# Optimization experiments

Hardware: AMD Instinct MI355X
Metric: run time of the kernel (lower is better)

## Reference

```python
import jax, jax.numpy as jnp
import numpy as np

H, KVH, HD = 32, 8, 128          # query heads, kv heads, head_dim
HIDDEN = H * HD                   # 4096
TOTAL_KV = 3072                   # sum of (start_pos + seqlen) over the batch (static)
ROPE_THETA = 10000.0


def setup_inputs() -> dict:
    key = jax.random.key(0)
    ks = jax.random.split(key, 4)
    x = jax.random.normal(ks[0], (1024, HIDDEN), jnp.float32)
    wqkv = jax.random.normal(ks[1], (HIDDEN, HIDDEN + 2 * KVH * HD), jnp.float32) * 0.02
    wo = jax.random.normal(ks[2], (HIDDEN, HIDDEN), jnp.float32) * 0.02
    # paged cache: [num_layers=1, 2(k/v), cache_slots, kv_heads, head_dim], holds post-RoPE prefixes
    kv_cache = jax.random.normal(ks[3], (1, 2, 8192, KVH, HD), jnp.float32) * 0.02
    # 4 ragged requests: seqlens [512,256,128,128], cached prefixes [0,512,1024,512]
    seqstarts = jnp.array([0, 512, 768, 896, 1024], jnp.int32)
    start_pos = jnp.array([0, 512, 1024, 512], jnp.int32)
    kvstarts = jnp.array([0, 512, 1280, 2432, 3072], jnp.int32)  # cumsum of start_pos+seqlen
    cachestarts = jnp.array([0, 1024, 2560, 4096], jnp.int32)    # page base per request
    return dict(x=x, wqkv=wqkv, wo=wo, kv_cache=kv_cache, seqstarts=seqstarts,
                kvstarts=kvstarts, cachestarts=cachestarts, start_pos=start_pos)


def _rope(t, pos):
    # interleaved (GPT-J style) rotary over full head_dim; t: [T, nheads, HD], pos: [T]
    d2 = HD // 2
    inv_freq = 1.0 / (ROPE_THETA ** (jnp.arange(d2, dtype=jnp.float32) / d2))
    ang = pos.astype(jnp.float32)[:, None] * inv_freq      # [T, d2]
    cos = jnp.cos(ang)[:, None, :]
    sin = jnp.sin(ang)[:, None, :]
    x1, x2 = t[..., 0::2], t[..., 1::2]
    r1 = x1 * cos - x2 * sin
    r2 = x1 * sin + x2 * cos
    return jnp.stack([r1, r2], axis=-1).reshape(t.shape)


def _forward(x, wqkv, wo, kv_cache, seqstarts, kvstarts, cachestarts, start_pos):
    T = x.shape[0]
    # fused QKV projection
    xqkv = (x @ wqkv).reshape(T, H + 2 * KVH, HD)
    xq, xk, xv = jnp.split(xqkv, [H, H + KVH], axis=1)   # [T,32,HD],[T,8,HD],[T,8,HD]

    # per-token batch id and absolute position (ragged via seqstarts)
    tok = jnp.arange(T)
    bq = jnp.searchsorted(seqstarts, tok, side='right') - 1
    pos_q = tok - seqstarts[bq] + start_pos[bq]
    xq = _rope(xq, pos_q)
    xk = _rope(xk, pos_q)

    # assemble ragged KV stream: cached prefix (paged cache) + freshly projected tokens
    kvtok = jnp.arange(TOTAL_KV)
    bkv = jnp.searchsorted(kvstarts, kvtok, side='right') - 1
    pkv = kvtok - kvstarts[bkv]                              # absolute kv position
    is_new = pkv >= start_pos[bkv]
    new_idx = jnp.clip(seqstarts[bkv] + pkv - start_pos[bkv], 0, T - 1)
    cache_idx = cachestarts[bkv] + pkv                       # paged slot for prefix
    keys = jnp.where(is_new[:, None, None], xk[new_idx], kv_cache[0, 0][cache_idx])
    vals = jnp.where(is_new[:, None, None], xv[new_idx], kv_cache[0, 1][cache_idx])

    # GQA: repeat kv heads to match query heads
    rep = H // KVH
    keys = jnp.repeat(keys, rep, axis=1)                     # [TOTAL_KV, 32, HD]
    vals = jnp.repeat(vals, rep, axis=1)

    scale = 1.0 / jnp.sqrt(jnp.float32(HD))
    scores = jnp.einsum('qhd,khd->hqk', xq, keys) * scale    # [32, T, TOTAL_KV]
    # ragged causal mask: same request and kv position <= query position
    mask = (bq[:, None] == bkv[None, :]) & (pkv[None, :] <= pos_q[:, None])
    scores = jnp.where(mask[None], scores, jnp.float32(-1e30))
    probs = jax.nn.softmax(scores, axis=-1)
    attn = jnp.einsum('hqk,khd->qhd', probs, vals)           # [T, 32, HD]
    return attn.reshape(T, HIDDEN) @ wo


def reference(x, wqkv, wo, kv_cache, seqstarts, kvstarts, cachestarts, start_pos):
    return _forward(x, wqkv, wo, kv_cache, seqstarts, kvstarts, cachestarts, start_pos)
```

## Files before the change

### kernel.cpp

```cpp
#include <hip/hip_runtime.h>
#include <hip/hip_bf16.h>
#include <math.h>
#include <stdint.h>

typedef __bf16 bf16;
typedef __attribute__((ext_vector_type(4))) float floatx4;
typedef __attribute__((ext_vector_type(8))) bf16 bf16x8;
typedef __attribute__((ext_vector_type(4))) bf16 bf16x4;

#define LDS_ASYNC16(gptr, lptr)                                                \
  __builtin_amdgcn_global_load_lds(                                            \
      (const __attribute__((address_space(1))) void*)(gptr),                   \
      (__attribute__((address_space(3))) void*)(lptr), 16, 0, 0)

__global__ __launch_bounds__(256) void k_merge(const float* __restrict__ a,
                                               const float* __restrict__ b,
                                               float* __restrict__ out) {
  int i = (blockIdx.x * 256 + threadIdx.x) * 4;
  float4 va = *(const float4*)(a + i);
  float4 vb = *(const float4*)(b + i);
  float4 o;
  o.x = va.x + vb.x; o.y = va.y + vb.y; o.z = va.z + vb.z; o.w = va.w + vb.w;
  *(float4*)(out + i) = o;
}

__device__ __forceinline__ void transpose_tile(const float* __restrict__ in,
                                               bf16* __restrict__ out, int K,
                                               int N, int bx, int by, int tid,
                                               float (*tile)[65]) {
  int k0 = by * 64, n0 = bx * 64;
  int cg = tid & 15, rr = tid >> 4;
#pragma unroll
  for (int p = 0; p < 4; ++p) {
    int r = rr + p * 16;
    float4 v = *(const float4*)(in + (size_t)(k0 + r) * N + n0 + cg * 4);
    tile[r][cg * 4 + 0] = v.x; tile[r][cg * 4 + 1] = v.y;
    tile[r][cg * 4 + 2] = v.z; tile[r][cg * 4 + 3] = v.w;
  }
  __syncthreads();
  int kc = tid & 7;
#pragma unroll
  for (int p = 0; p < 2; ++p) {
    int n = (tid >> 3) + p * 32;
    bf16x8 o;
#pragma unroll
    for (int e = 0; e < 8; ++e) o[e] = (bf16)tile[kc * 8 + e][n];
    *(bf16x8*)(out + (size_t)(n0 + n) * K + k0 + kc * 8) = o;
  }
}

__global__ __launch_bounds__(256) void k_prep(const float* __restrict__ x,
                                              const float* __restrict__ wqkv,
                                              const float* __restrict__ wo,
                                              bf16* __restrict__ x_bf,
                                              bf16* __restrict__ wqkvT,
                                              bf16* __restrict__ woT) {
  __shared__ float tile[64][65];
  int bid = blockIdx.x, tid = threadIdx.x;
  if (bid < 2048) {
    int i = (bid * 256 + tid) * 8;
    float4 a = *(const float4*)(x + i);
    float4 b = *(const float4*)(x + i + 4);
    bf16x8 o;
    o[0] = (bf16)a.x; o[1] = (bf16)a.y; o[2] = (bf16)a.z; o[3] = (bf16)a.w;
    o[4] = (bf16)b.x; o[5] = (bf16)b.y; o[6] = (bf16)b.z; o[7] = (bf16)b.w;
    *(bf16x8*)(x_bf + i) = o;
  } else if (bid < 8192) {
    int q = bid - 2048;
    transpose_tile(wqkv, wqkvT, 4096, 6144, q >> 6, q & 63, tid, tile);
  } else {
    int q = bid - 8192;
    transpose_tile(wo, woT, 4096, 4096, q >> 6, q & 63, tid, tile);
  }
}

__global__ __launch_bounds__(256) void k_gemm_bt(const bf16* __restrict__ A,
                                                 const bf16* __restrict__ B,
                                                 float* __restrict__ C,
                                                 int M, int N, int K, int ksplit) {
  __shared__ bf16 As[128 * 32];
  __shared__ bf16 Bs[128 * 32];
  int tid = threadIdx.x;
  int w = tid >> 6, lane = tid & 63;
  int lq = lane >> 4, l16 = lane & 15;
  int bm = blockIdx.y * 128, bn = blockIdx.x * 128;
  int wm = (w >> 1) * 64, wn = (w & 1) * 64;
  int kc = K / ksplit;
  int koff = blockIdx.z * kc;
  C += (size_t)blockIdx.z * M * N;
  floatx4 acc[4][4] = {};
  const bf16* Ab = A + (size_t)bm * K;
  const bf16* Bb = B + (size_t)bn * K;
  int srow = (lane >> 2);
  int scol = (((lane & 3) ^ ((srow >> 1) & 3))) * 8;
  int sa = (l16 >> 1) & 3;

  for (int k0 = koff; k0 < koff + kc; k0 += 32) {
#pragma unroll
    for (int c = 0; c < 2; ++c) {
      int r = w * 32 + c * 16 + srow;
      LDS_ASYNC16(Ab + (size_t)r * K + k0 + scol, &As[(w * 32 + c * 16) * 32]);
      LDS_ASYNC16(Bb + (size_t)r * K + k0 + scol, &Bs[(w * 32 + c * 16) * 32]);
    }
    __syncthreads();
    bf16x8 af[4], bfr[4];
#pragma unroll
    for (int i = 0; i < 4; ++i)
      af[i] = *(const bf16x8*)&As[(wm + i * 16 + l16) * 32 + (lq ^ sa) * 8];
#pragma unroll
    for (int j = 0; j < 4; ++j)
      bfr[j] = *(const bf16x8*)&Bs[(wn + j * 16 + l16) * 32 + (lq ^ sa) * 8];
#pragma unroll
    for (int i = 0; i < 4; ++i)
#pragma unroll
      for (int j = 0; j < 4; ++j)
        acc[i][j] = __builtin_amdgcn_mfma_f32_16x16x32_bf16(af[i], bfr[j],
                                                            acc[i][j], 0, 0, 0);
    __syncthreads();
  }
#pragma unroll
  for (int i = 0; i < 4; ++i)
#pragma unroll
    for (int j = 0; j < 4; ++j) {
      int m = bm + wm + i * 16 + lq * 4;
      int n = bn + wn + j * 16 + l16;
      float* cp = C + (size_t)m * N + n;
#pragma unroll
      for (int r = 0; r < 4; ++r) cp[(size_t)r * N] = acc[i][j][r];
    }
}

__global__ __launch_bounds__(256) void k_rope_asm(
    const float* __restrict__ xp0, const float* __restrict__ xp1,
    bf16* __restrict__ qb, bf16* __restrict__ kall, bf16* __restrict__ vT,
    const float* __restrict__ ck, const float* __restrict__ cv,
    const int* __restrict__ seqstarts, const int* __restrict__ kvstarts,
    const int* __restrict__ cachestarts, const int* __restrict__ start_pos) {
  __shared__ float tile[64][130];
  int bid = blockIdx.x, tid = threadIdx.x;
  if (bid < 1024) {
    int t = bid;
    int s = 0;
    for (int i = 1; i < 4; ++i) if (seqstarts[i] <= t) s = i;
    int posn = t - seqstarts[s] + start_pos[s];
    float pos = (float)posn;
    int krow = kvstarts[s] + posn;
    for (int wk = tid; wk < 40 * 64; wk += 256) {
      int hh = wk >> 6, j = wk & 63;
      size_t idx = ((size_t)t * 48 + hh) * 128 + 2 * j;
      float2 a0 = *(const float2*)(xp0 + idx);
      float2 a1 = *(const float2*)(xp1 + idx);
      float x1 = a0.x + a1.x;
      float x2 = a0.y + a1.y;
      float invf = exp2f(-(float)j * 0.20762050593045935f);
      float ang = pos * invf;
      float sv, cv2;
      sincosf(ang, &sv, &cv2);
      float r1 = x1 * cv2 - x2 * sv;
      float r2 = x1 * sv + x2 * cv2;
      unsigned int u1 = (unsigned int)__builtin_bit_cast(unsigned short, (bf16)r1);
      unsigned int u2 = (unsigned int)__builtin_bit_cast(unsigned short, (bf16)r2);
      unsigned int pk = u1 | (u2 << 16);
      unsigned int* dst = (hh < 32)
          ? (unsigned int*)(qb + ((size_t)t * 32 + hh) * 128)
          : (unsigned int*)(kall + ((size_t)(hh - 32) * 3072 + krow) * 128);
      dst[j] = pk;
    }
    return;
  }
  int rb = bid - 1024;
  if (rb < 3072) {
    int p = rb;
    int b = 0;
    for (int i = 1; i < 4; ++i) if (kvstarts[i] <= p) b = i;
    int pkv = p - kvstarts[b];
    if (pkv >= start_pos[b]) return;
    int hk = tid >> 5, d4 = (tid & 31) * 4;
    int ci = cachestarts[b] + pkv;
    float4 v = *(const float4*)(ck + ((size_t)ci * 8 + hk) * 128 + d4);
    bf16x4 o;
    o[0] = (bf16)v.x; o[1] = (bf16)v.y; o[2] = (bf16)v.z; o[3] = (bf16)v.w;
    *(bf16x4*)(kall + ((size_t)hk * 3072 + p) * 128 + d4) = o;
    return;
  }
  int q = rb - 3072;
  int hk = q / 48, p0 = (q % 48) * 64;
  {
    int r = tid >> 2;
    int p = p0 + r;
    int b = 0;
    for (int i = 1; i < 4; ++i) if (kvstarts[i] <= p) b = i;
    int pkv = p - kvstarts[b];
    int f0 = (tid & 3) * 32;
    if (pkv >= start_pos[b]) {
      int tn = seqstarts[b] + pkv - start_pos[b];
      size_t base = (size_t)tn * 6144 + (40 + hk) * 128;
#pragma unroll
      for (int i = 0; i < 8; ++i) {
        float4 v0 = *(const float4*)(xp0 + base + f0 + i * 4);
        float4 v1 = *(const float4*)(xp1 + base + f0 + i * 4);
        tile[r][f0 + i * 4 + 0] = v0.x + v1.x;
        tile[r][f0 + i * 4 + 1] = v0.y + v1.y;
        tile[r][f0 + i * 4 + 2] = v0.z + v1.z;
        tile[r][f0 + i * 4 + 3] = v0.w + v1.w;
      }
    } else {
      int ci = cachestarts[b] + pkv;
      const float* src = cv + ((size_t)ci * 8 + hk) * 128;
#pragma unroll
      for (int i = 0; i < 8; ++i) {
        float4 v = *(const float4*)(src + f0 + i * 4);
        tile[r][f0 + i * 4 + 0] = v.x; tile[r][f0 + i * 4 + 1] = v.y;
        tile[r][f0 + i * 4 + 2] = v.z; tile[r][f0 + i * 4 + 3] = v.w;
      }
    }
  }
  __syncthreads();
  int d = tid >> 1, hf = tid & 1;
  bf16* dst = vT + ((size_t)hk * 128 + d) * 3072 + p0 + hf * 32;
#pragma unroll
  for (int qq = 0; qq < 4; ++qq) {
    bf16x8 o;
#pragma unroll
    for (int e = 0; e < 8; ++e) o[e] = (bf16)tile[hf * 32 + qq * 8 + e][d];
    *(bf16x8*)(dst + qq * 8) = o;
  }
}

__global__ __launch_bounds__(256) void k_attn(
    const bf16* __restrict__ qb, const bf16* __restrict__ kall,
    const bf16* __restrict__ vT, bf16* __restrict__ aout,
    const int* __restrict__ seqstarts, const int* __restrict__ kvstarts,
    const int* __restrict__ start_pos) {
  __shared__ bf16 Ks[64 * 128];
  __shared__ bf16 Vs[128 * 64];
  __shared__ bf16 Ps[64 * 64];
  int bid = blockIdx.x;
  int half = bid >> 8, idx = bid & 255;
  int h = half * 16 + (idx >> 4);
  int qbi = half ? (idx & 15) : 15 - (idx & 15);
  int hk = h >> 2;
  int t0 = qbi * 64;
  int s = 0;
  for (int i = 1; i < 4; ++i) if (seqstarts[i] <= t0) s = i;
  int posbase = t0 - seqstarts[s] + start_pos[s];
  int kv0 = kvstarts[s];
  int nkv = posbase + 64;
  int tid = threadIdx.x, w = tid >> 6, lane = tid & 63;
  int lq = lane >> 4, l16 = lane & 15;

  bf16x8 qa[4];
#pragma unroll
  for (int kk = 0; kk < 4; ++kk)
    qa[kk] = *(const bf16x8*)(qb + (((size_t)(t0 + w * 16 + l16) * 32 + h) * 128 +
                                    kk * 32 + lq * 8));

  int krow = lane >> 4;
  int vrow = lane >> 3;
  int vchunk = ((lane & 7) ^ (vrow & 7));
  int sw8 = l16 & 7;

  float m_r[4], l_r[4];
  floatx4 oacc[8] = {};
#pragma unroll
  for (int rg = 0; rg < 4; ++rg) { m_r[rg] = -3.0e38f; l_r[rg] = 0.f; }
  const float scale = 0.08838834764831845f;

  for (int p0 = 0; p0 < nkv; p0 += 64) {
#pragma unroll
    for (int c = 0; c < 4; ++c) {
      int base_r = w * 16 + c * 4;
      int r = base_r + krow;
      int gch = (lane & 15) ^ ((c * 4 + krow) & 15);
      LDS_ASYNC16(kall + (((size_t)hk * 3072 + kv0 + p0 + r) * 128 + gch * 8),
                  &Ks[base_r * 128]);
    }
#pragma unroll
    for (int c = 0; c < 4; ++c) {
      int base_d = w * 32 + c * 8;
      int d = base_d + vrow;
      LDS_ASYNC16(vT + (((size_t)hk * 128 + d) * 3072 + kv0 + p0 + vchunk * 8),
                  &Vs[base_d * 64]);
    }
    __syncthreads();

    floatx4 sacc[4] = {};
#pragma unroll
    for (int kk = 0; kk < 4; ++kk)
#pragma unroll
      for (int j = 0; j < 4; ++j) {
        bf16x8 kb = *(const bf16x8*)&Ks[(j * 16 + l16) * 128 +
                                        ((kk * 4 + lq) ^ l16) * 8];
        sacc[j] = __builtin_amdgcn_mfma_f32_16x16x32_bf16(qa[kk], kb, sacc[j], 0, 0, 0);
      }

#pragma unroll
    for (int rg = 0; rg < 4; ++rg) {
      int qpos = posbase + w * 16 + lq * 4 + rg;
      float sv[4];
      float rmax = -3.0e38f;
#pragma unroll
      for (int j = 0; j < 4; ++j) {
        int pkv = p0 + j * 16 + l16;
        sv[j] = (pkv <= qpos) ? sacc[j][rg] * scale : -3.0e38f;
        rmax = fmaxf(rmax, sv[j]);
      }
#pragma unroll
      for (int off = 1; off < 16; off <<= 1)
        rmax = fmaxf(rmax, __shfl_xor(rmax, off, 64));
      float mnew = fmaxf(m_r[rg], rmax);
      float alpha = __expf(m_r[rg] - mnew);
      m_r[rg] = mnew;
      int prow = w * 16 + lq * 4 + rg;
      int pswz = (lq * 4 + rg) & 7;
      float psum = 0.f;
#pragma unroll
      for (int j = 0; j < 4; ++j) {
        float pv = __expf(sv[j] - mnew);
        psum += pv;
        int chunk = (j * 2 + (l16 >> 3)) ^ pswz;
        Ps[prow * 64 + chunk * 8 + (l16 & 7)] = (bf16)pv;
      }
#pragma unroll
      for (int off = 1; off < 16; off <<= 1) psum += __shfl_xor(psum, off, 64);
      l_r[rg] = l_r[rg] * alpha + psum;
#pragma unroll
      for (int nt = 0; nt < 8; ++nt) oacc[nt][rg] *= alpha;
    }

#pragma unroll
    for (int kk = 0; kk < 2; ++kk) {
      bf16x8 pa = *(const bf16x8*)&Ps[(w * 16 + l16) * 64 +
                                      ((kk * 4 + lq) ^ sw8) * 8];
#pragma unroll
      for (int nt = 0; nt < 8; ++nt) {
        bf16x8 vb = *(const bf16x8*)&Vs[(nt * 16 + l16) * 64 +
                                        ((kk * 4 + lq) ^ sw8) * 8];
        oacc[nt] = __builtin_amdgcn_mfma_f32_16x16x32_bf16(pa, vb, oacc[nt], 0, 0, 0);
      }
    }
    __syncthreads();
  }

#pragma unroll
  for (int rg = 0; rg < 4; ++rg) {
    int row = w * 16 + lq * 4 + rg;
    float inv = 1.0f / l_r[rg];
    bf16* dst = aout + (size_t)(t0 + row) * 4096 + h * 128;
#pragma unroll
    for (int nt = 0; nt < 8; ++nt)
      dst[nt * 16 + l16] = (bf16)(oacc[nt][rg] * inv);
  }
}

extern "C" void kernel_launch(void* const* d_in, const int* in_sizes, int n_in,
                              void* d_out, int out_size, void* d_ws, size_t ws_size,
                              hipStream_t stream) {
  const float* x = (const float*)d_in[0];
  const float* wqkv = (const float*)d_in[1];
  const float* wo = (const float*)d_in[2];
  const float* kv = (const float*)d_in[3];
  const int* seqstarts = (const int*)d_in[4];
  const int* kvstarts = (const int*)d_in[5];
  const int* cachestarts = (const int*)d_in[6];
  const int* start_pos = (const int*)d_in[7];
  float* out = (float*)d_out;

  char* base = (char*)d_ws;
  size_t off = 0;
  auto carve = [&](size_t bytes) {
    void* r = base + off;
    off += (bytes + 255) & ~(size_t)255;
    return r;
  };
  bf16* x_bf    = (bf16*)carve(1024ull * 4096 * 2);
  bf16* wqkvT   = (bf16*)carve(6144ull * 4096 * 2);
  bf16* woT     = (bf16*)carve(4096ull * 4096 * 2);
  float* xqkv   = (float*)carve(2ull * 1024 * 6144 * 4);
  bf16* q_bf    = (bf16*)carve(1024ull * 32 * 128 * 2);
  bf16* k_all   = (bf16*)carve(8ull * 3072 * 128 * 2);
  bf16* vT_all  = (bf16*)carve(8ull * 128 * 3072 * 2);
  bf16* attn_bf = (bf16*)carve(1024ull * 4096 * 2);
  float* outp = (float*)wqkvT;

  float* xqkv1 = xqkv + 1024ull * 6144;
  const float* cache_v = kv + 8192ull * 8 * 128;

  k_prep<<<12288, 256, 0, stream>>>(x, wqkv, wo, x_bf, wqkvT, woT);
  k_gemm_bt<<<dim3(48, 8, 2), 256, 0, stream>>>(x_bf, wqkvT, xqkv, 1024, 6144,
                                                4096, 2);
  k_rope_asm<<<4480, 256, 0, stream>>>(xqkv, xqkv1, q_bf, k_all, vT_all, kv,
                                       cache_v, seqstarts, kvstarts,
                                       cachestarts, start_pos);
  k_attn<<<512, 256, 0, stream>>>(q_bf, k_all, vT_all, attn_bf,
                                  seqstarts, kvstarts, start_pos);
  k_gemm_bt<<<dim3(32, 8, 2), 256, 0, stream>>>(attn_bf, woT, outp, 1024, 4096,
                                                4096, 2);
  k_merge<<<4096, 256, 0, stream>>>(outp, outp + 1024ull * 4096, out);
}
```

Measured before the change: 474.8 us.

## Widen weight transpose tiles and split attention into 32-row query blocks

The weight transpose in the prep kernel now handles 64x128 tiles per block, with all global loads batched into registers before the LDS writes and narrower bf16x4 stores on the way out. The attention kernel drops to 128 threads (2 waves) per block over 32-query tiles, doubling the grid to 1024 blocks and reordering them so heavy query tiles start first. This aims for better load balance and occupancy in attention and fewer, larger transpose blocks. The risks are that the narrower bf16x4 stores coalesce less well, and that each block now loads the full K/V tiles for only 32 queries, so K/V reuse per block halves.

Result: no change. 474.9 us (+0.0%).

```diff
diff --git a/kernel.cpp b/kernel.cpp
--- a/kernel.cpp
+++ b/kernel.cpp
@@ -24,28 +24,38 @@
   *(float4*)(out + i) = o;
 }
 
-__device__ __forceinline__ void transpose_tile(const float* __restrict__ in,
-                                               bf16* __restrict__ out, int K,
-                                               int N, int bx, int by, int tid,
-                                               float (*tile)[65]) {
-  int k0 = by * 64, n0 = bx * 64;
+__device__ __forceinline__ void transpose_tile128(const float* __restrict__ in,
+                                                  bf16* __restrict__ out, int K,
+                                                  int N, int bx, int by, int tid,
+                                                  float (*tile)[129]) {
+  int k0 = by * 64, n0 = bx * 128;
   int cg = tid & 15, rr = tid >> 4;
-#pragma unroll
-  for (int p = 0; p < 4; ++p) {
-    int r = rr + p * 16;
-    float4 v = *(const float4*)(in + (size_t)(k0 + r) * N + n0 + cg * 4);
-    tile[r][cg * 4 + 0] = v.x; tile[r][cg * 4 + 1] = v.y;
-    tile[r][cg * 4 + 2] = v.z; tile[r][cg * 4 + 3] = v.w;
-  }
+  float4 v[8];
+#pragma unroll
+  for (int p = 0; p < 4; ++p)
+#pragma unroll
+    for (int h = 0; h < 2; ++h)
+      v[p * 2 + h] = *(const float4*)(in + (size_t)(k0 + rr + p * 16) * N +
+                                      n0 + h * 64 + cg * 4);
+#pragma unroll
+  for (int p = 0; p < 4; ++p)
+#pragma unroll
+    for (int h = 0; h < 2; ++h) {
+      float4 t = v[p * 2 + h];
+      int r = rr + p * 16, c = h * 64 + cg * 4;
+      tile[r][c + 0] = t.x; tile[r][c + 1] = t.y;
+      tile[r][c + 2] = t.z; tile[r][c + 3] = t.w;
+    }
   __syncthreads();
-  int kc = tid & 7;
-#pragma unroll
-  for (int p = 0; p < 2; ++p) {
-    int n = (tid >> 3) + p * 32;
-    bf16x8 o;
-#pragma unroll
-    for (int e = 0; e < 8; ++e) o[e] = (bf16)tile[kc * 8 + e][n];
-    *(bf16x8*)(out + (size_t)(n0 + n) * K + k0 + kc * 8) = o;
+#pragma unroll
+  for (int p = 0; p < 8; ++p) {
+    int n = rr + p * 16;
+    bf16x4 o;
+    o[0] = (bf16)tile[cg * 4 + 0][n];
+    o[1] = (bf16)tile[cg * 4 + 1][n];
+    o[2] = (bf16)tile[cg * 4 + 2][n];
+    o[3] = (bf16)tile[cg * 4 + 3][n];
+    *(bf16x4*)(out + (size_t)(n0 + n) * K + k0 + cg * 4) = o;
   }
 }
 
@@ -55,7 +65,7 @@
                                               bf16* __restrict__ x_bf,
                                               bf16* __restrict__ wqkvT,
                                               bf16* __restrict__ woT) {
-  __shared__ float tile[64][65];
+  __shared__ float tile[64][129];
   int bid = blockIdx.x, tid = threadIdx.x;
   if (bid < 2048) {
     int i = (bid * 256 + tid) * 8;
@@ -65,12 +75,12 @@
     o[0] = (bf16)a.x; o[1] = (bf16)a.y; o[2] = (bf16)a.z; o[3] = (bf16)a.w;
     o[4] = (bf16)b.x; o[5] = (bf16)b.y; o[6] = (bf16)b.z; o[7] = (bf16)b.w;
     *(bf16x8*)(x_bf + i) = o;
-  } else if (bid < 8192) {
+  } else if (bid < 5120) {
     int q = bid - 2048;
-    transpose_tile(wqkv, wqkvT, 4096, 6144, q >> 6, q & 63, tid, tile);
+    transpose_tile128(wqkv, wqkvT, 4096, 6144, q >> 6, q & 63, tid, tile);
   } else {
-    int q = bid - 8192;
-    transpose_tile(wo, woT, 4096, 4096, q >> 6, q & 63, tid, tile);
+    int q = bid - 5120;
+    transpose_tile128(wo, woT, 4096, 4096, q >> 6, q & 63, tid, tile);
   }
 }
 
@@ -227,25 +237,24 @@
   }
 }
 
-__global__ __launch_bounds__(256) void k_attn(
+__global__ __launch_bounds__(128) void k_attn(
     const bf16* __restrict__ qb, const bf16* __restrict__ kall,
     const bf16* __restrict__ vT, bf16* __restrict__ aout,
     const int* __restrict__ seqstarts, const int* __restrict__ kvstarts,
     const int* __restrict__ start_pos) {
   __shared__ bf16 Ks[64 * 128];
   __shared__ bf16 Vs[128 * 64];
-  __shared__ bf16 Ps[64 * 64];
+  __shared__ bf16 Ps[32 * 64];
   int bid = blockIdx.x;
-  int half = bid >> 8, idx = bid & 255;
-  int h = half * 16 + (idx >> 4);
-  int qbi = half ? (idx & 15) : 15 - (idx & 15);
+  int h = bid & 31;
+  int q32 = (24 + (bid >> 5)) & 31;
   int hk = h >> 2;
-  int t0 = qbi * 64;
+  int t0 = q32 * 32;
   int s = 0;
   for (int i = 1; i < 4; ++i) if (seqstarts[i] <= t0) s = i;
   int posbase = t0 - seqstarts[s] + start_pos[s];
   int kv0 = kvstarts[s];
-  int nkv = posbase + 64;
+  int nkv = posbase + 32;
   int tid = threadIdx.x, w = tid >> 6, lane = tid & 63;
   int lq = lane >> 4, l16 = lane & 15;
 
@@ -268,16 +277,16 @@
 
   for (int p0 = 0; p0 < nkv; p0 += 64) {
 #pragma unroll
-    for (int c = 0; c < 4; ++c) {
-      int base_r = w * 16 + c * 4;
+    for (int c = 0; c < 8; ++c) {
+      int base_r = w * 32 + c * 4;
       int r = base_r + krow;
       int gch = (lane & 15) ^ ((c * 4 + krow) & 15);
       LDS_ASYNC16(kall + (((size_t)hk * 3072 + kv0 + p0 + r) * 128 + gch * 8),
                   &Ks[base_r * 128]);
     }
 #pragma unroll
-    for (int c = 0; c < 4; ++c) {
-      int base_d = w * 32 + c * 8;
+    for (int c = 0; c < 8; ++c) {
+      int base_d = w * 64 + c * 8;
       int d = base_d + vrow;
       LDS_ASYNC16(vT + (((size_t)hk * 128 + d) * 3072 + kv0 + p0 + vchunk * 8),
                   &Vs[base_d * 64]);
@@ -386,14 +395,14 @@
   float* xqkv1 = xqkv + 1024ull * 6144;
   const float* cache_v = kv + 8192ull * 8 * 128;
 
-  k_prep<<<12288, 256, 0, stream>>>(x, wqkv, wo, x_bf, wqkvT, woT);
+  k_prep<<<7168, 256, 0, stream>>>(x, wqkv, wo, x_bf, wqkvT, woT);
   k_gemm_bt<<<dim3(48, 8, 2), 256, 0, stream>>>(x_bf, wqkvT, xqkv, 1024, 6144,
                                                 4096, 2);
   k_rope_asm<<<4480, 256, 0, stream>>>(xqkv, xqkv1, q_bf, k_all, vT_all, kv,
                                        cache_v, seqstarts, kvstarts,
                                        cachestarts, start_pos);
-  k_attn<<<512, 256, 0, stream>>>(q_bf, k_all, vT_all, attn_bf,
-                                  seqstarts, kvstarts, start_pos);
+  k_attn<<<1024, 128, 0, stream>>>(q_bf, k_all, vT_all, attn_bf,
+                                   seqstarts, kvstarts, start_pos);
   k_gemm_bt<<<dim3(32, 8, 2), 256, 0, stream>>>(attn_bf, woT, outp, 1024, 4096,
                                                 4096, 2);
   k_merge<<<4096, 256, 0, stream>>>(outp, outp + 1024ull * 4096, out);
```
